# Kernel tuning notes

Hardware: AMD Instinct MI355X
Metric: run time of the kernel (lower is better)

## Reference

```python
import jax, jax.numpy as jnp
import numpy as np

B, T = 65536, 200
H, S, P = 512, 1000, 5
EPS = 1e-6


def setup_inputs() -> dict:
    key = jax.random.key(0)
    ks = jax.random.split(key, 8)
    init = lambda k, shp, fan: (jax.random.normal(k, shp, jnp.float32) / np.float32(np.sqrt(fan)))
    return {
        "X": jax.random.randint(ks[0], (B,), 0, S, dtype=jnp.int32),
        "y": jax.random.randint(ks[1], (B, T), 0, 2, dtype=jnp.int32),
        "embed": init(ks[2], (S, H), 1.0),
        "W1": init(ks[3], (H, H), H), "b1": jnp.zeros((H,), jnp.float32),
        "W2": init(ks[4], (H, H), H), "b2": jnp.zeros((H,), jnp.float32),
        "Wout": init(ks[5], (H, P), H), "bout": jnp.zeros((P,), jnp.float32),
    }


def reference(X, y, embed, W1, b1, W2, b2, Wout, bout):
    # --- MLP over skill embeddings: params (B, 5) = (l, f, g, s, latent0) ---
    e = embed[X]                                    # (B, H)
    h = jax.nn.relu(e @ W1 + b1)                    # num_layers = 2
    h = jax.nn.relu(h @ W2 + b2)
    params = jnp.clip(jax.nn.sigmoid(h @ Wout + bout), EPS, 1.0 - EPS)  # (B, 5)
    l, g, s = params[:, 0], params[:, 2], params[:, 3]
    latent0 = params[:, 4]                          # (B,)

    y_clean = jnp.where(y == -1, 0, y).astype(jnp.float32)  # (B, T)

    # --- BKT latent-update recurrence over T steps ---
    def step(latent, y_t):
        num1 = latent * (1.0 - s)
        correct = num1 + (1.0 - latent) * g
        k_t1 = num1 / correct
        k_t0 = latent * s / (latent * s + (1.0 - latent) * (1.0 - g))
        k_t = jnp.where(y_t > 0.5, k_t1, k_t0)
        nxt = jnp.clip(k_t + (1.0 - k_t) * l, EPS, 1.0 - EPS)
        return nxt, (correct, latent)

    _, (corrects, latents) = jax.lax.scan(step, latent0, y_clean.T)  # (T, B) each
    return corrects.T, latents.T, params
```

## Files before the change

kernel.cpp:

```cpp
#include <hip/hip_runtime.h>


typedef unsigned int uint;
typedef unsigned short ushort_t;
typedef __attribute__((ext_vector_type(8))) short short8;
typedef __attribute__((ext_vector_type(4))) float f32x4;

#define SS 1000
#define HH 512
#define TT 200
#define BB_ 65536
#define PP 5

#define OFF_EMB   0
#define OFF_W1    512000
#define OFF_B1    774144
#define OFF_W2    774656
#define OFF_B2    1036800
#define OFF_WOUT  1037312
#define OFF_BOUT  1039872
#define CONV_TOT  1039877

__device__ __forceinline__ float b2f(ushort_t u) {
    return __uint_as_float(((uint)u) << 16);
}
__device__ __forceinline__ ushort_t f2b(float f) {
    uint u = __float_as_uint(f);
    uint r = u + 0x7FFFu + ((u >> 16) & 1u);
    return (ushort_t)(r >> 16);
}

__global__ void detect_dtype(const uint* __restrict__ embed_raw,
                             int* __restrict__ flag) {
    int lane = threadIdx.x;
    uint w = embed_raw[lane];
    uint e = (w >> 7) & 0xFFu;
    bool plaus = (e >= 117u && e <= 130u);
    unsigned long long m = __ballot(plaus);
    if (lane == 0) flag[0] = (__popcll(m) >= 32) ? 1 : 0;
}

__global__ __launch_bounds__(256) void convert_inputs(
    const void* __restrict__ embed, const void* __restrict__ W1,
    const void* __restrict__ b1,    const void* __restrict__ W2,
    const void* __restrict__ b2,    const void* __restrict__ Wout,
    const void* __restrict__ bout,  const int* __restrict__ flag,
    ushort_t* __restrict__ dst)
{
    int i = blockIdx.x * 256 + threadIdx.x;
    if (i >= CONV_TOT) return;
    const void* src; int off;
    if      (i < OFF_W1)   { src = embed; off = i; }
    else if (i < OFF_B1)   { src = W1;    off = i - OFF_W1; }
    else if (i < OFF_W2)   { src = b1;    off = i - OFF_B1; }
    else if (i < OFF_B2)   { src = W2;    off = i - OFF_W2; }
    else if (i < OFF_WOUT) { src = b2;    off = i - OFF_B2; }
    else if (i < OFF_BOUT) { src = Wout;  off = i - OFF_WOUT; }
    else                   { src = bout;  off = i - OFF_BOUT; }
    ushort_t v;
    if (flag[0]) v = ((const ushort_t*)src)[off];
    else         v = f2b(((const float*)src)[off]);
    dst[i] = v;
}

__global__ __launch_bounds__(256) void transpose_w(
    const ushort_t* __restrict__ conv, ushort_t* __restrict__ WT1,
    ushort_t* __restrict__ WT2)
{
    __shared__ ushort_t t[32][33];
    const ushort_t* W = conv + (blockIdx.z ? OFF_W2 : OFF_W1);
    ushort_t* WT = blockIdx.z ? WT2 : WT1;
    int k0 = blockIdx.x * 32, n0 = blockIdx.y * 32;
    int tx = threadIdx.x, ty = threadIdx.y;
    for (int i = ty; i < 32; i += 8)
        t[i][tx] = W[(k0 + i) * HH + n0 + tx];
    __syncthreads();
    for (int i = ty; i < 32; i += 8)
        WT[(n0 + i) * HH + k0 + tx] = t[tx][i];
}

__global__ __launch_bounds__(256) void mlp_layer(
    const ushort_t* __restrict__ A, const ushort_t* __restrict__ WT,
    const ushort_t* __restrict__ bias, ushort_t* __restrict__ H, int Mclamp)
{
    int tid = threadIdx.x;
    int lane = tid & 63;
    int wave = tid >> 6;
    int m_base = blockIdx.x * 64 + wave * 16;
    int n_base = blockIdx.y * 64;
    int lrow = lane & 15;
    int q = lane >> 4;
    int rowA = m_base + lrow; if (rowA > Mclamp) rowA = Mclamp;

    const short8* Ap  = (const short8*)(A + (size_t)rowA * HH) + q;
    const short8* Bp0 = (const short8*)(WT + (size_t)(n_base + 0 * 16 + lrow) * HH) + q;
    const short8* Bp1 = (const short8*)(WT + (size_t)(n_base + 1 * 16 + lrow) * HH) + q;
    const short8* Bp2 = (const short8*)(WT + (size_t)(n_base + 2 * 16 + lrow) * HH) + q;
    const short8* Bp3 = (const short8*)(WT + (size_t)(n_base + 3 * 16 + lrow) * HH) + q;

    f32x4 acc0 = {0.f,0.f,0.f,0.f}, acc1 = {0.f,0.f,0.f,0.f};
    f32x4 acc2 = {0.f,0.f,0.f,0.f}, acc3 = {0.f,0.f,0.f,0.f};

    #pragma unroll 4
    for (int kk = 0; kk < 16; kk++) {
        short8 a  = Ap[kk * 4];
        short8 b0 = Bp0[kk * 4];
        short8 b1v = Bp1[kk * 4];
        short8 b2v = Bp2[kk * 4];
        short8 b3v = Bp3[kk * 4];
        acc0 = __builtin_amdgcn_mfma_f32_16x16x32_bf16(a, b0,  acc0, 0, 0, 0);
        acc1 = __builtin_amdgcn_mfma_f32_16x16x32_bf16(a, b1v, acc1, 0, 0, 0);
        acc2 = __builtin_amdgcn_mfma_f32_16x16x32_bf16(a, b2v, acc2, 0, 0, 0);
        acc3 = __builtin_amdgcn_mfma_f32_16x16x32_bf16(a, b3v, acc3, 0, 0, 0);
    }

    int orow = m_base + q * 4;
    f32x4 accs[4] = {acc0, acc1, acc2, acc3};
    #pragma unroll
    for (int nt = 0; nt < 4; nt++) {
        int n = n_base + nt * 16 + lrow;
        float bb = b2f(bias[n]);
        #pragma unroll
        for (int r = 0; r < 4; r++) {
            float v = accs[nt][r] + bb;
            H[(size_t)(orow + r) * HH + n] = f2b(fmaxf(v, 0.f));
        }
    }
}

__global__ __launch_bounds__(256) void params_kernel(
    const ushort_t* __restrict__ h2, const ushort_t* __restrict__ conv,
    float* __restrict__ table)
{
    int wid = blockIdx.x * 4 + (threadIdx.x >> 6);
    int lane = threadIdx.x & 63;
    if (wid >= SS * PP) return;
    int row = wid / PP, p = wid - row * PP;
    const ushort_t* Wout = conv + OFF_WOUT;
    const ushort_t* bout = conv + OFF_BOUT;
    const short8* hr = (const short8*)(h2 + (size_t)row * HH);
    short8 h = hr[lane];
    float acc = 0.f;
    #pragma unroll
    for (int j = 0; j < 8; j++) {
        int k = lane * 8 + j;
        acc += b2f((ushort_t)h[j]) * b2f(Wout[k * PP + p]);
    }
    #pragma unroll
    for (int m = 32; m; m >>= 1) acc += __shfl_xor(acc, m);
    if (lane == 0) {
        float x = acc + b2f(bout[p]);
        float sg = 1.f / (1.f + expf(-x));
        sg = fminf(fmaxf(sg, 1e-6f), 1.f - 1e-6f);
        table[(size_t)row * 8 + p] = sg;
    }
}

__global__ __launch_bounds__(64) void scan_kernel(
    const int* __restrict__ X, const int* __restrict__ y,
    const float* __restrict__ table, const int* __restrict__ flag,
    void* __restrict__ out)
{
    __shared__ uint y_su[64 * 11];
    __shared__ uint cs[64 * 41];
    __shared__ uint lsb[64 * 41];
    int tid = threadIdx.x;
    int b0 = blockIdx.x * 64;
    int b = b0 + tid;
    int fb = flag[0];
    int xi = X[b]; xi = xi < 0 ? 0 : (xi >= SS ? SS - 1 : xi);
    float l      = table[xi * 8 + 0];
    float p1     = table[xi * 8 + 1];
    float g      = table[xi * 8 + 2];
    float s      = table[xi * 8 + 3];
    float latent = table[xi * 8 + 4];

    if (fb) {
        ushort_t* pout = (ushort_t*)out + 2ull * BB_ * TT + (size_t)b * 5;
        pout[0] = f2b(l); pout[1] = f2b(p1); pout[2] = f2b(g);
        pout[3] = f2b(s); pout[4] = f2b(latent);
    } else {
        float* pout = (float*)out + 2ull * BB_ * TT + (size_t)b * 5;
        pout[0] = l; pout[1] = p1; pout[2] = g; pout[3] = s; pout[4] = latent;
    }

    char* cgb = (char*)out;
    char* lgb = (char*)out + (fb ? 2ull : 4ull) * BB_ * TT;
    float oms = 1.f - s, omg = 1.f - g;

    for (int chunk = 0; chunk < 5; chunk++) {
        int c0 = chunk * 40;
        __syncthreads();
        #pragma unroll
        for (int k2 = 0; k2 < 10; k2++) {
            int gix = tid + k2 * 64;
            int r = gix / 10, q2 = gix - r * 10;
            int4 v = *(const int4*)(y + (size_t)(b0 + r) * TT + c0 + q2 * 4);
            uint pk = (uint)(v.x == 1) | ((uint)(v.y == 1) << 8) |
                      ((uint)(v.z == 1) << 16) | ((uint)(v.w == 1) << 24);
            y_su[r * 11 + q2] = pk;
        }
        __syncthreads();
        #pragma unroll
        for (int j4 = 0; j4 < 10; j4++) {
            uint u = y_su[tid * 11 + j4];
            float cv[4], lv[4];
            #pragma unroll
            for (int i = 0; i < 4; i++) {
                float num1    = latent * oms;
                float correct = num1 + (1.f - latent) * g;
                float lat_s   = latent * s;
                bool yt = (u >> (8 * i)) & 1u;
                float num = yt ? num1 : lat_s;
                float den = yt ? correct : (lat_s + (1.f - latent) * omg);
                float kt = num / den;
                cv[i] = correct;
                lv[i] = latent;
                float nxt = kt + (1.f - kt) * l;
                latent = fminf(fmaxf(nxt, 1e-6f), 1.f - 1e-6f);
            }
            if (fb) {
                cs[tid * 41 + j4 * 2]      = (uint)f2b(cv[0]) | ((uint)f2b(cv[1]) << 16);
                cs[tid * 41 + j4 * 2 + 1]  = (uint)f2b(cv[2]) | ((uint)f2b(cv[3]) << 16);
                lsb[tid * 41 + j4 * 2]     = (uint)f2b(lv[0]) | ((uint)f2b(lv[1]) << 16);
                lsb[tid * 41 + j4 * 2 + 1] = (uint)f2b(lv[2]) | ((uint)f2b(lv[3]) << 16);
            } else {
                #pragma unroll
                for (int i = 0; i < 4; i++) {
                    cs[tid * 41 + j4 * 4 + i]  = __float_as_uint(cv[i]);
                    lsb[tid * 41 + j4 * 4 + i] = __float_as_uint(lv[i]);
                }
            }
        }
        __syncthreads();
        if (fb) {
            #pragma unroll
            for (int k2 = 0; k2 < 20; k2++) {
                int gix = tid + k2 * 64;
                int r = gix / 20, q2 = gix - r * 20;
                size_t off = (size_t)(b0 + r) * 400 + (size_t)c0 * 2 + q2 * 4;
                *(uint*)(cgb + off) = cs[r * 41 + q2];
                *(uint*)(lgb + off) = lsb[r * 41 + q2];
            }
        } else {
            #pragma unroll
            for (int k2 = 0; k2 < 40; k2++) {
                int gix = tid + k2 * 64;
                int r = gix / 40, q2 = gix - r * 40;
                size_t off = (size_t)(b0 + r) * 800 + (size_t)c0 * 4 + q2 * 4;
                *(uint*)(cgb + off) = cs[r * 41 + q2];
                *(uint*)(lgb + off) = lsb[r * 41 + q2];
            }
        }
    }
}

extern "C" void kernel_launch(void* const* d_in, const int* in_sizes, int n_in,
                              void* d_out, int out_size, void* d_ws, size_t ws_size,
                              hipStream_t stream) {
    const int* X = (const int*)d_in[0];
    const int* y = (const int*)d_in[1];

    char* ws = (char*)d_ws;
    ushort_t* conv  = (ushort_t*)(ws);
    ushort_t* WT1   = (ushort_t*)(ws + 2097152);
    ushort_t* WT2   = (ushort_t*)(ws + 2621440);
    ushort_t* h1    = (ushort_t*)(ws + 3145728);
    ushort_t* h2    = (ushort_t*)(ws + 4194304);
    float*    table = (float*)(ws + 5242880);
    int*      flag  = (int*)(ws + 5275648);

    detect_dtype<<<1, 64, 0, stream>>>((const uint*)d_in[2], flag);
    convert_inputs<<<(CONV_TOT + 255) / 256, 256, 0, stream>>>(
        d_in[2], d_in[3], d_in[4], d_in[5], d_in[6], d_in[7], d_in[8],
        flag, conv);
    transpose_w<<<dim3(16, 16, 2), dim3(32, 8, 1), 0, stream>>>(conv, WT1, WT2);
    mlp_layer<<<dim3(16, 8, 1), 256, 0, stream>>>(conv + OFF_EMB, WT1, conv + OFF_B1, h1, SS - 1);
    mlp_layer<<<dim3(16, 8, 1), 256, 0, stream>>>(h1, WT2, conv + OFF_B2, h2, 1023);
    params_kernel<<<dim3(1250, 1, 1), 256, 0, stream>>>(h2, conv, table);
    scan_kernel<<<dim3(BB_ / 64, 1, 1), 64, 0, stream>>>(X, y, table, flag, (void*)d_out);
}
```

Baseline: 247.7 us.

## Fuse prep kernels, preload y bits, and simplify scan arithmetic

Merges dtype detection, input conversion and weight transpose into a single prep kernel, and has each kernel recompute the dtype flag inline instead of reading it from workspace. This removes two launches and an intermediate copy of W1/W2. The scan kernel now loads all 200 y values per row up front as 4-bit packed bytes, where it used to reload them per chunk. The recurrence uses algebraically merged FMAs and a hardware reciprocal instead of a division, and stores go out with 8-byte writes in the fp32 path. The approximate reciprocal may change the results slightly, and holding all of y in shared memory changes the load pattern.

```diff
diff --git a/kernel.cpp b/kernel.cpp
--- a/kernel.cpp
+++ b/kernel.cpp
@@ -2,6 +2,7 @@
 
 
 typedef unsigned int uint;
+typedef unsigned char uchar;
 typedef unsigned short ushort_t;
 typedef __attribute__((ext_vector_type(8))) short short8;
 typedef __attribute__((ext_vector_type(4))) float f32x4;
@@ -13,13 +14,11 @@
 #define PP 5
 
 #define OFF_EMB   0
-#define OFF_W1    512000
-#define OFF_B1    774144
-#define OFF_W2    774656
-#define OFF_B2    1036800
-#define OFF_WOUT  1037312
-#define OFF_BOUT  1039872
-#define CONV_TOT  1039877
+#define OFF_B1    512000
+#define OFF_B2    512512
+#define OFF_WOUT  513024
+#define OFF_BOUT  515584
+#define CONV_TOT  515589
 
 __device__ __forceinline__ float b2f(ushort_t u) {
     return __uint_as_float(((uint)u) << 16);
@@ -29,54 +28,55 @@
     uint r = u + 0x7FFFu + ((u >> 16) & 1u);
     return (ushort_t)(r >> 16);
 }
-
-__global__ void detect_dtype(const uint* __restrict__ embed_raw,
-                             int* __restrict__ flag) {
-    int lane = threadIdx.x;
-    uint w = embed_raw[lane];
+__device__ __forceinline__ int detect_bf16(const uint* __restrict__ embed_raw,
+                                           int tid) {
+    uint w = embed_raw[tid & 63];
     uint e = (w >> 7) & 0xFFu;
-    bool plaus = (e >= 117u && e <= 130u);
-    unsigned long long m = __ballot(plaus);
-    if (lane == 0) flag[0] = (__popcll(m) >= 32) ? 1 : 0;
-}
-
-__global__ __launch_bounds__(256) void convert_inputs(
+    bool pl = (e >= 117u && e <= 130u);
+    return __popcll(__ballot(pl)) >= 32 ? 1 : 0;
+}
+__device__ __forceinline__ ushort_t ld_bf16(const void* src, int idx, int fb) {
+    return fb ? ((const ushort_t*)src)[idx] : f2b(((const float*)src)[idx]);
+}
+
+__global__ __launch_bounds__(256) void prep_kernel(
     const void* __restrict__ embed, const void* __restrict__ W1,
     const void* __restrict__ b1,    const void* __restrict__ W2,
     const void* __restrict__ b2,    const void* __restrict__ Wout,
-    const void* __restrict__ bout,  const int* __restrict__ flag,
-    ushort_t* __restrict__ dst)
-{
-    int i = blockIdx.x * 256 + threadIdx.x;
-    if (i >= CONV_TOT) return;
-    const void* src; int off;
-    if      (i < OFF_W1)   { src = embed; off = i; }
-    else if (i < OFF_B1)   { src = W1;    off = i - OFF_W1; }
-    else if (i < OFF_W2)   { src = b1;    off = i - OFF_B1; }
-    else if (i < OFF_B2)   { src = W2;    off = i - OFF_W2; }
-    else if (i < OFF_WOUT) { src = b2;    off = i - OFF_B2; }
-    else if (i < OFF_BOUT) { src = Wout;  off = i - OFF_WOUT; }
-    else                   { src = bout;  off = i - OFF_BOUT; }
-    ushort_t v;
-    if (flag[0]) v = ((const ushort_t*)src)[off];
-    else         v = f2b(((const float*)src)[off]);
-    dst[i] = v;
-}
-
-__global__ __launch_bounds__(256) void transpose_w(
-    const ushort_t* __restrict__ conv, ushort_t* __restrict__ WT1,
+    const void* __restrict__ bout,
+    ushort_t* __restrict__ conv, ushort_t* __restrict__ WT1,
     ushort_t* __restrict__ WT2)
 {
-    __shared__ ushort_t t[32][33];
-    const ushort_t* W = conv + (blockIdx.z ? OFF_W2 : OFF_W1);
-    ushort_t* WT = blockIdx.z ? WT2 : WT1;
-    int k0 = blockIdx.x * 32, n0 = blockIdx.y * 32;
-    int tx = threadIdx.x, ty = threadIdx.y;
-    for (int i = ty; i < 32; i += 8)
-        t[i][tx] = W[(k0 + i) * HH + n0 + tx];
-    __syncthreads();
-    for (int i = ty; i < 32; i += 8)
-        WT[(n0 + i) * HH + k0 + tx] = t[tx][i];
+    int tid = threadIdx.x;
+    int fb = detect_bf16((const uint*)embed, tid);
+    int bx = blockIdx.x;
+    if (bx < 2015) {
+        int i = bx * 256 + tid;
+        if (i < CONV_TOT) {
+            const void* src; int off;
+            if      (i < OFF_B1)   { src = embed; off = i; }
+            else if (i < OFF_B2)   { src = b1;    off = i - OFF_B1; }
+            else if (i < OFF_WOUT) { src = b2;    off = i - OFF_B2; }
+            else if (i < OFF_BOUT) { src = Wout;  off = i - OFF_WOUT; }
+            else                   { src = bout;  off = i - OFF_BOUT; }
+            conv[i] = ld_bf16(src, off, fb);
+        }
+    } else {
+        __shared__ ushort_t t[32][33];
+        int bi = bx - 2015;
+        const void* W = bi < 256 ? W1 : W2;
+        ushort_t* WT = bi < 256 ? WT1 : WT2;
+        int ti = bi & 255;
+        int k0 = (ti & 15) * 32, n0 = (ti >> 4) * 32;
+        int tx = tid & 31, ty = tid >> 5;
+        #pragma unroll
+        for (int i = ty; i < 32; i += 8)
+            t[i][tx] = ld_bf16(W, (k0 + i) * HH + n0 + tx, fb);
+        __syncthreads();
+        #pragma unroll
+        for (int i = ty; i < 32; i += 8)
+            WT[(n0 + i) * HH + k0 + tx] = t[tx][i];
+    }
 }
 
 __global__ __launch_bounds__(256) void mlp_layer(
@@ -103,8 +103,8 @@
 
     #pragma unroll 4
     for (int kk = 0; kk < 16; kk++) {
-        short8 a  = Ap[kk * 4];
-        short8 b0 = Bp0[kk * 4];
+        short8 a   = Ap[kk * 4];
+        short8 b0  = Bp0[kk * 4];
         short8 b1v = Bp1[kk * 4];
         short8 b2v = Bp2[kk * 4];
         short8 b3v = Bp3[kk * 4];
@@ -158,16 +158,25 @@
 
 __global__ __launch_bounds__(64) void scan_kernel(
     const int* __restrict__ X, const int* __restrict__ y,
-    const float* __restrict__ table, const int* __restrict__ flag,
+    const float* __restrict__ table, const uint* __restrict__ embed_raw,
     void* __restrict__ out)
 {
-    __shared__ uint y_su[64 * 11];
-    __shared__ uint cs[64 * 41];
-    __shared__ uint lsb[64 * 41];
+    __shared__ uchar yb[64 * 52];
+    __shared__ __align__(16) uint stg[2][64 * 42];
     int tid = threadIdx.x;
     int b0 = blockIdx.x * 64;
     int b = b0 + tid;
-    int fb = flag[0];
+    int fb = detect_bf16(embed_raw, tid);
+
+    #pragma unroll
+    for (int k2 = 0; k2 < 50; k2++) {
+        int gix = tid + k2 * 64;
+        int r = gix / 50, q = gix - r * 50;
+        int4 v = *(const int4*)(y + (size_t)(b0 + r) * TT + q * 4);
+        yb[r * 52 + q] = (uchar)((uint)(v.x == 1) | ((uint)(v.y == 1) << 1) |
+                                 ((uint)(v.z == 1) << 2) | ((uint)(v.w == 1) << 3));
+    }
+
     int xi = X[b]; xi = xi < 0 ? 0 : (xi >= SS ? SS - 1 : xi);
     float l      = table[xi * 8 + 0];
     float p1     = table[xi * 8 + 1];
@@ -186,72 +195,71 @@
 
     char* cgb = (char*)out;
     char* lgb = (char*)out + (fb ? 2ull : 4ull) * BB_ * TT;
-    float oms = 1.f - s, omg = 1.f - g;
-
-    for (int chunk = 0; chunk < 5; chunk++) {
-        int c0 = chunk * 40;
-        __syncthreads();
-        #pragma unroll
-        for (int k2 = 0; k2 < 10; k2++) {
-            int gix = tid + k2 * 64;
-            int r = gix / 10, q2 = gix - r * 10;
-            int4 v = *(const int4*)(y + (size_t)(b0 + r) * TT + c0 + q2 * 4);
-            uint pk = (uint)(v.x == 1) | ((uint)(v.y == 1) << 8) |
-                      ((uint)(v.z == 1) << 16) | ((uint)(v.w == 1) << 24);
-            y_su[r * 11 + q2] = pk;
-        }
-        __syncthreads();
+    float oms = 1.f - s;
+    float omg = 1.f - g;
+    float A1  = 1.f - s - g;
+    float A0  = s + g - 1.f;
+    float oml = 1.f - l;
+
+    __syncthreads();
+
+    for (int c = 0; c < 5; c++) {
         #pragma unroll
         for (int j4 = 0; j4 < 10; j4++) {
-            uint u = y_su[tid * 11 + j4];
-            float cv[4], lv[4];
+            uint u = yb[tid * 52 + c * 10 + j4];
+            uint pc0 = 0, pc1 = 0, pl0 = 0, pl1 = 0;
             #pragma unroll
             for (int i = 0; i < 4; i++) {
                 float num1    = latent * oms;
-                float correct = num1 + (1.f - latent) * g;
-                float lat_s   = latent * s;
-                bool yt = (u >> (8 * i)) & 1u;
-                float num = yt ? num1 : lat_s;
-                float den = yt ? correct : (lat_s + (1.f - latent) * omg);
-                float kt = num / den;
-                cv[i] = correct;
-                lv[i] = latent;
-                float nxt = kt + (1.f - kt) * l;
+                float correct = fmaf(latent, A1, g);
+                float lats    = latent * s;
+                bool yt = (u >> i) & 1u;
+                float num = yt ? num1 : lats;
+                float den = yt ? correct : fmaf(latent, A0, omg);
+                float kt  = num * __builtin_amdgcn_rcpf(den);
+                if (!fb) {
+                    stg[0][tid * 42 + j4 * 4 + i] = __float_as_uint(correct);
+                    stg[1][tid * 42 + j4 * 4 + i] = __float_as_uint(latent);
+                } else {
+                    uint cb = (uint)f2b(correct), lb = (uint)f2b(latent);
+                    if (i == 0)      { pc0 = cb;        pl0 = lb; }
+                    else if (i == 1) { pc0 |= cb << 16; pl0 |= lb << 16; }
+                    else if (i == 2) { pc1 = cb;        pl1 = lb; }
+                    else             { pc1 |= cb << 16; pl1 |= lb << 16; }
+                }
+                float nxt = fmaf(kt, oml, l);
                 latent = fminf(fmaxf(nxt, 1e-6f), 1.f - 1e-6f);
             }
             if (fb) {
-                cs[tid * 41 + j4 * 2]      = (uint)f2b(cv[0]) | ((uint)f2b(cv[1]) << 16);
-                cs[tid * 41 + j4 * 2 + 1]  = (uint)f2b(cv[2]) | ((uint)f2b(cv[3]) << 16);
-                lsb[tid * 41 + j4 * 2]     = (uint)f2b(lv[0]) | ((uint)f2b(lv[1]) << 16);
-                lsb[tid * 41 + j4 * 2 + 1] = (uint)f2b(lv[2]) | ((uint)f2b(lv[3]) << 16);
-            } else {
-                #pragma unroll
-                for (int i = 0; i < 4; i++) {
-                    cs[tid * 41 + j4 * 4 + i]  = __float_as_uint(cv[i]);
-                    lsb[tid * 41 + j4 * 4 + i] = __float_as_uint(lv[i]);
-                }
+                stg[0][tid * 21 + j4 * 2]     = pc0;
+                stg[0][tid * 21 + j4 * 2 + 1] = pc1;
+                stg[1][tid * 21 + j4 * 2]     = pl0;
+                stg[1][tid * 21 + j4 * 2 + 1] = pl1;
             }
         }
         __syncthreads();
-        if (fb) {
+        if (!fb) {
             #pragma unroll
             for (int k2 = 0; k2 < 20; k2++) {
                 int gix = tid + k2 * 64;
-                int r = gix / 20, q2 = gix - r * 20;
-                size_t off = (size_t)(b0 + r) * 400 + (size_t)c0 * 2 + q2 * 4;
-                *(uint*)(cgb + off) = cs[r * 41 + q2];
-                *(uint*)(lgb + off) = lsb[r * 41 + q2];
+                int r = gix / 20, q = gix - r * 20;
+                uint2 vc = *(const uint2*)&stg[0][r * 42 + q * 2];
+                uint2 vl = *(const uint2*)&stg[1][r * 42 + q * 2];
+                size_t off = (size_t)(b0 + r) * 800 + (size_t)c * 160 + q * 8;
+                *(uint2*)(cgb + off) = vc;
+                *(uint2*)(lgb + off) = vl;
             }
         } else {
             #pragma unroll
-            for (int k2 = 0; k2 < 40; k2++) {
+            for (int k2 = 0; k2 < 10; k2++) {
                 int gix = tid + k2 * 64;
-                int r = gix / 40, q2 = gix - r * 40;
-                size_t off = (size_t)(b0 + r) * 800 + (size_t)c0 * 4 + q2 * 4;
-                *(uint*)(cgb + off) = cs[r * 41 + q2];
-                *(uint*)(lgb + off) = lsb[r * 41 + q2];
-            }
-        }
+                int r = gix / 10, q = gix - r * 10;
+                size_t off = (size_t)(b0 + r) * 400 + (size_t)c * 80 + q * 4;
+                *(uint*)(cgb + off) = stg[0][r * 21 + q];
+                *(uint*)(lgb + off) = stg[1][r * 21 + q];
+            }
+        }
+        __syncthreads();
     }
 }
 
@@ -263,20 +271,18 @@
 
     char* ws = (char*)d_ws;
     ushort_t* conv  = (ushort_t*)(ws);
-    ushort_t* WT1   = (ushort_t*)(ws + 2097152);
-    ushort_t* WT2   = (ushort_t*)(ws + 2621440);
-    ushort_t* h1    = (ushort_t*)(ws + 3145728);
-    ushort_t* h2    = (ushort_t*)(ws + 4194304);
-    float*    table = (float*)(ws + 5242880);
-    int*      flag  = (int*)(ws + 5275648);
-
-    detect_dtype<<<1, 64, 0, stream>>>((const uint*)d_in[2], flag);
-    convert_inputs<<<(CONV_TOT + 255) / 256, 256, 0, stream>>>(
+    ushort_t* WT1   = (ushort_t*)(ws + 1048576);
+    ushort_t* WT2   = (ushort_t*)(ws + 1572864);
+    ushort_t* h1    = (ushort_t*)(ws + 2097152);
+    ushort_t* h2    = (ushort_t*)(ws + 3145728);
+    float*    table = (float*)(ws + 4194304);
+
+    prep_kernel<<<dim3(2527, 1, 1), 256, 0, stream>>>(
         d_in[2], d_in[3], d_in[4], d_in[5], d_in[6], d_in[7], d_in[8],
-        flag, conv);
-    transpose_w<<<dim3(16, 16, 2), dim3(32, 8, 1), 0, stream>>>(conv, WT1, WT2);
+        conv, WT1, WT2);
     mlp_layer<<<dim3(16, 8, 1), 256, 0, stream>>>(conv + OFF_EMB, WT1, conv + OFF_B1, h1, SS - 1);
     mlp_layer<<<dim3(16, 8, 1), 256, 0, stream>>>(h1, WT2, conv + OFF_B2, h2, 1023);
     params_kernel<<<dim3(1250, 1, 1), 256, 0, stream>>>(h2, conv, table);
-    scan_kernel<<<dim3(BB_ / 64, 1, 1), 64, 0, stream>>>(X, y, table, flag, (void*)d_out);
-}
+    scan_kernel<<<dim3(BB_ / 64, 1, 1), 64, 0, stream>>>(
+        X, y, table, (const uint*)d_in[2], (void*)d_out);
+}
```

After: 218.7 us. 11.7% less time.
